# Kernel tuning notes

Hardware: AMD Instinct MI355X
Metric: run time of the kernel (lower is better)

Reference implementation:

```python
import jax, jax.numpy as jnp
import numpy as np

D_MODEL = 1024
N_HEADS = 16
N_KV = 4
HEAD_DIM = 64
R = 256
B, N = 2, 2048


def setup_inputs() -> dict:
    key = jax.random.key(0)
    ks = jax.random.split(key, 5)
    x = jax.random.normal(ks[0], (B, N, D_MODEL), jnp.float32)
    # rotary cos/sin table: (N, HEAD_DIM//2, 2)
    inv = 1.0 / (10000.0 ** (jnp.arange(0, HEAD_DIM, 2, dtype=jnp.float32) / HEAD_DIM))
    ang = jnp.arange(N, dtype=jnp.float32)[:, None] * inv[None, :]
    freqs_cis = jnp.stack([jnp.cos(ang), jnp.sin(ang)], axis=-1)
    s = 0.02
    Wq = jax.random.normal(ks[1], (D_MODEL, N_HEADS * HEAD_DIM), jnp.float32) * s
    Wk = jax.random.normal(ks[2], (D_MODEL, N_KV * HEAD_DIM), jnp.float32) * s
    Wv = jax.random.normal(ks[3], (D_MODEL, N_KV * HEAD_DIM), jnp.float32) * s
    Wo = jax.random.normal(ks[4], (N_HEADS * HEAD_DIM, D_MODEL), jnp.float32) * s
    return dict(x=x, freqs_cis=freqs_cis, Wq=Wq, Wk=Wk, Wv=Wv, Wo=Wo)


def _select_pairs(scores_i, best_b_i, r):
    """Greedy top-r pair selection with unique-b constraint (one batch row)."""
    half = scores_i.shape[0]
    order = jnp.argsort(-scores_i)  # descending by best similarity

    def step(carry, a_local):
        used, count = carry
        b_local = best_b_i[a_local]
        take = jnp.logical_and(jnp.logical_not(used[b_local]), count < r)
        used = used.at[b_local].set(used[b_local] | take)
        count = count + take.astype(jnp.int32)
        return (used, count), (take, a_local.astype(jnp.int32), b_local.astype(jnp.int32))

    (_, count), (takes, a_locs, b_locs) = jax.lax.scan(
        step, (jnp.zeros(half, bool), jnp.int32(0)), order)
    pos = jnp.cumsum(takes.astype(jnp.int32)) - 1
    idx = jnp.where(takes, pos, r)  # dump non-taken into slot r
    sel_a = jnp.zeros(r + 1, jnp.int32).at[idx].set(a_locs)[:r]
    sel_b = jnp.zeros(r + 1, jnp.int32).at[idx].set(b_locs)[:r]
    valid = jnp.arange(r) < count  # pad (if fewer than r unique) with first pair
    sel_a = jnp.where(valid, sel_a, sel_a[0])
    sel_b = jnp.where(valid, sel_b, sel_b[0])
    return sel_a, sel_b


def bipartite_indices(metric, r):
    """Returns (global_a, global_b, keep_idx) for merge/unmerge."""
    Bm, Nm, _ = metric.shape
    a = metric[:, 0::2]  # (B, half, C)
    b = metric[:, 1::2]
    an = a / jnp.maximum(jnp.linalg.norm(a, axis=-1, keepdims=True), 1e-12)
    bn = b / jnp.maximum(jnp.linalg.norm(b, axis=-1, keepdims=True), 1e-12)
    scores = jnp.einsum('bic,bjc->bij', an, bn)  # (B, half, half)
    best_scores = scores.max(axis=2)
    best_b = scores.argmax(axis=2)
    sel_a, sel_b = jax.vmap(lambda s, m: _select_pairs(s, m, r))(best_scores, best_b)
    global_a = 2 * sel_a      # even indices
    global_b = 2 * sel_b + 1  # odd indices
    bidx = jnp.arange(Bm)[:, None]
    keep_mask = jnp.ones((Bm, Nm), bool).at[bidx, global_b].set(False)
    # stable argsort puts kept (False) positions first, in original order
    keep_idx = jnp.argsort(~keep_mask, axis=1)[:, :Nm - r]
    return global_a, global_b, keep_idx


def merge(x, global_a, global_b, keep_idx):
    Bm = x.shape[0]
    bidx = jnp.arange(Bm)[:, None]
    xa = jnp.take_along_axis(x, global_a[..., None], axis=1)
    xb = jnp.take_along_axis(x, global_b[..., None], axis=1)
    x_out = x.at[bidx, global_a].set((xa + xb) * 0.5)
    return jnp.take_along_axis(x_out, keep_idx[..., None], axis=1)


def unmerge(xm, global_a, global_b, keep_idx, n_orig):
    Bm, _, C = xm.shape
    bidx = jnp.arange(Bm)[:, None]
    out = jnp.zeros((Bm, n_orig, C), xm.dtype).at[bidx, keep_idx].set(xm)
    xa = jnp.take_along_axis(out, global_a[..., None], axis=1)
    return out.at[bidx, global_b].set(xa)


def _rope(t, freqs):
    # t: (B, N, H, HD), freqs: (N, HD//2, 2)
    cos = freqs[None, :, None, :, 0]
    sin = freqs[None, :, None, :, 1]
    t1 = t[..., 0::2]
    t2 = t[..., 1::2]
    rot = jnp.stack([t1 * cos - t2 * sin, t1 * sin + t2 * cos], axis=-1)
    return rot.reshape(t.shape)


def _attention(x_m, freqs, Wq, Wk, Wv, Wo):
    Bm, Nm, _ = x_m.shape
    q = (x_m @ Wq).reshape(Bm, Nm, N_HEADS, HEAD_DIM)
    k = (x_m @ Wk).reshape(Bm, Nm, N_KV, HEAD_DIM)
    v = (x_m @ Wv).reshape(Bm, Nm, N_KV, HEAD_DIM)
    q = _rope(q, freqs)
    k = _rope(k, freqs)
    rep = N_HEADS // N_KV
    k = jnp.repeat(k, rep, axis=2)
    v = jnp.repeat(v, rep, axis=2)
    att = jnp.einsum('bqhd,bkhd->bhqk', q, k) / np.sqrt(HEAD_DIM).astype(np.float32)
    w = jax.nn.softmax(att, axis=-1)
    o = jnp.einsum('bhqk,bkhd->bqhd', w, v).reshape(Bm, Nm, N_HEADS * HEAD_DIM)
    return o @ Wo


def reference(x, freqs_cis, Wq, Wk, Wv, Wo):
    n = x.shape[1]
    metric = jax.lax.stop_gradient(x @ Wk)  # k_proj under no_grad
    ga, gb, ki = bipartite_indices(metric, R)
    x_m = merge(x, ga, gb, ki)
    n_merged = x_m.shape[1]
    out_m = _attention(x_m, freqs_cis[:n_merged], Wq, Wk, Wv, Wo)
    return unmerge(out_m, ga, gb, ki, n)
```

## Files before the change

### kernel.cpp

```cpp
#include <hip/hip_runtime.h>
#include <hip/hip_bf16.h>
#include <math.h>

#define BB 2
#define NN 2048
#define DM 1024
#define NH 16
#define NKV 4
#define HD 64
#define RR 256
#define HALF 1024
#define NM 1792
#define NT 28
#define NSPL 4

typedef __bf16 bf16x8 __attribute__((ext_vector_type(8)));
typedef float f32x4 __attribute__((ext_vector_type(4)));

__device__ inline unsigned pk2(float a, float b) {
  union { __bf16 h; unsigned short u; } ua, ub;
  ua.h = (__bf16)a;
  ub.h = (__bf16)b;
  return (unsigned)ua.u | ((unsigned)ub.u << 16);
}

__device__ inline unsigned shu(unsigned v, int s) {
  return (unsigned)__shfl((int)v, s, 64);
}

__device__ __forceinline__ void async16(const void* g, void* l) {
  __builtin_amdgcn_global_load_lds(
      (const __attribute__((address_space(1))) void*)g,
      (__attribute__((address_space(3))) void*)l, 16, 0, 0);
}

__global__ __launch_bounds__(256) void gemm_bf16(
    const __bf16* __restrict__ A, const __bf16* __restrict__ Bt,
    float* __restrict__ C, int M, int N, int K) {
  __shared__ __align__(16) __bf16 As[8192];
  __shared__ __align__(16) __bf16 Bs[4096];
  const int bm0 = blockIdx.x * 128;
  const int bn0 = blockIdx.y * 64;
  const int w = threadIdx.x >> 6;
  const int lane = threadIdx.x & 63;
  f32x4 acc[2][4];
#pragma unroll
  for (int i = 0; i < 2; ++i)
#pragma unroll
    for (int nt = 0; nt < 4; ++nt) acc[i][nt] = (f32x4){0.f, 0.f, 0.f, 0.f};
  for (int kk = 0; kk < K; kk += 64) {
    __syncthreads();
#pragma unroll
    for (int it = 0; it < 4; ++it) {
      const int c = it * 256 + w * 64 + lane;
      async16(A + (size_t)(bm0 + ((c >> 7) << 4) + (c & 15)) * K + kk +
                  (((c >> 6) & 1) << 5) + (((c >> 4) & 3) << 3),
              &As[(it * 256 + w * 64) * 8]);
    }
#pragma unroll
    for (int it = 0; it < 2; ++it) {
      const int c = it * 256 + w * 64 + lane;
      async16(Bt + (size_t)(bn0 + ((c >> 7) << 4) + (c & 15)) * K + kk +
                  (((c >> 6) & 1) << 5) + (((c >> 4) & 3) << 3),
              &Bs[(it * 256 + w * 64) * 8]);
    }
    __syncthreads();
#pragma unroll
    for (int s = 0; s < 2; ++s) {
      bf16x8 a0 = *(const bf16x8*)&As[((2 * w) * 128 + s * 64 + lane) * 8];
      bf16x8 a1 = *(const bf16x8*)&As[((2 * w + 1) * 128 + s * 64 + lane) * 8];
#pragma unroll
      for (int nt = 0; nt < 4; ++nt) {
        bf16x8 bfr = *(const bf16x8*)&Bs[(nt * 128 + s * 64 + lane) * 8];
        acc[0][nt] =
            __builtin_amdgcn_mfma_f32_16x16x32_bf16(a0, bfr, acc[0][nt], 0, 0, 0);
        acc[1][nt] =
            __builtin_amdgcn_mfma_f32_16x16x32_bf16(a1, bfr, acc[1][nt], 0, 0, 0);
      }
    }
  }
  const int g = lane >> 4, ml = lane & 15;
#pragma unroll
  for (int i = 0; i < 2; ++i)
#pragma unroll
    for (int nt = 0; nt < 4; ++nt)
#pragma unroll
      for (int r = 0; r < 4; ++r)
        C[(size_t)(bm0 + (2 * w + i) * 16 + g * 4 + r) * N + bn0 + nt * 16 +
          ml] = acc[i][nt][r];
}

__global__ __launch_bounds__(256) void gemm_wo(
    const __bf16* __restrict__ A, const __bf16* __restrict__ Bt,
    const int* __restrict__ keep_idx, const int* __restrict__ dst2,
    float* __restrict__ out, int M, int N, int K) {
  __shared__ __align__(16) __bf16 As[8192];
  __shared__ __align__(16) __bf16 Bs[4096];
  const int bm0 = blockIdx.x * 128;
  const int bn0 = blockIdx.y * 64;
  const int w = threadIdx.x >> 6;
  const int lane = threadIdx.x & 63;
  f32x4 acc[2][4];
#pragma unroll
  for (int i = 0; i < 2; ++i)
#pragma unroll
    for (int nt = 0; nt < 4; ++nt) acc[i][nt] = (f32x4){0.f, 0.f, 0.f, 0.f};
  for (int kk = 0; kk < K; kk += 64) {
    __syncthreads();
#pragma unroll
    for (int it = 0; it < 4; ++it) {
      const int c = it * 256 + w * 64 + lane;
      async16(A + (size_t)(bm0 + ((c >> 7) << 4) + (c & 15)) * K + kk +
                  (((c >> 6) & 1) << 5) + (((c >> 4) & 3) << 3),
              &As[(it * 256 + w * 64) * 8]);
    }
#pragma unroll
    for (int it = 0; it < 2; ++it) {
      const int c = it * 256 + w * 64 + lane;
      async16(Bt + (size_t)(bn0 + ((c >> 7) << 4) + (c & 15)) * K + kk +
                  (((c >> 6) & 1) << 5) + (((c >> 4) & 3) << 3),
              &Bs[(it * 256 + w * 64) * 8]);
    }
    __syncthreads();
#pragma unroll
    for (int s = 0; s < 2; ++s) {
      bf16x8 a0 = *(const bf16x8*)&As[((2 * w) * 128 + s * 64 + lane) * 8];
      bf16x8 a1 = *(const bf16x8*)&As[((2 * w + 1) * 128 + s * 64 + lane) * 8];
#pragma unroll
      for (int nt = 0; nt < 4; ++nt) {
        bf16x8 bfr = *(const bf16x8*)&Bs[(nt * 128 + s * 64 + lane) * 8];
        acc[0][nt] =
            __builtin_amdgcn_mfma_f32_16x16x32_bf16(a0, bfr, acc[0][nt], 0, 0, 0);
        acc[1][nt] =
            __builtin_amdgcn_mfma_f32_16x16x32_bf16(a1, bfr, acc[1][nt], 0, 0, 0);
      }
    }
  }
  const int g = lane >> 4, ml = lane & 15;
#pragma unroll
  for (int i = 0; i < 2; ++i)
#pragma unroll
    for (int r = 0; r < 4; ++r) {
      const int row = bm0 + (2 * w + i) * 16 + g * 4 + r;
      const int bb = row / NM, tt = row % NM;
      const int p1 = keep_idx[bb * NM + tt];
      const int p2 = dst2[bb * NM + tt];
#pragma unroll
      for (int nt = 0; nt < 4; ++nt) {
        const int col = bn0 + nt * 16 + ml;
        float v = acc[i][nt][r];
        out[((size_t)(bb * NN + p1)) * DM + col] = v;
        if (p2 >= 0) out[((size_t)(bb * NN + p2)) * DM + col] = v;
      }
    }
}

__global__ __launch_bounds__(256) void gemm3t(
    const __bf16* __restrict__ Ah, const __bf16* __restrict__ Al,
    const __bf16* __restrict__ Bh, const __bf16* __restrict__ Bl,
    float* __restrict__ C0, float* __restrict__ C1, int M, int N, int K) {
  __shared__ __align__(16) __bf16 Ahs[4096], Als[4096], Bhs[4096], Bls[4096];
  const int z = blockIdx.z;
  float* C = z ? C1 : C0;
  const int kof = z * (K / 2);
  const int bm0 = blockIdx.x * 64;
  const int bn0 = blockIdx.y * 64;
  const int w = threadIdx.x >> 6;
  const int lane = threadIdx.x & 63;
  f32x4 acc[4];
#pragma unroll
  for (int nt = 0; nt < 4; ++nt) acc[nt] = (f32x4){0.f, 0.f, 0.f, 0.f};
  for (int kk = kof; kk < kof + K / 2; kk += 64) {
    __syncthreads();
#pragma unroll
    for (int it = 0; it < 2; ++it) {
      const int c = it * 256 + w * 64 + lane;
      const size_t ra = (size_t)(bm0 + ((c >> 7) << 4) + (c & 15)) * K;
      const size_t rb = (size_t)(bn0 + ((c >> 7) << 4) + (c & 15)) * K;
      const int col = kk + (((c >> 6) & 1) << 5) + (((c >> 4) & 3) << 3);
      const int lb = (it * 256 + w * 64) * 8;
      async16(Ah + ra + col, &Ahs[lb]);
      async16(Al + ra + col, &Als[lb]);
      async16(Bh + rb + col, &Bhs[lb]);
      async16(Bl + rb + col, &Bls[lb]);
    }
    __syncthreads();
#pragma unroll
    for (int s = 0; s < 2; ++s) {
      bf16x8 ah = *(const bf16x8*)&Ahs[((w * 2 + s) * 64 + lane) * 8];
      bf16x8 al = *(const bf16x8*)&Als[((w * 2 + s) * 64 + lane) * 8];
#pragma unroll
      for (int nt = 0; nt < 4; ++nt) {
        bf16x8 bh = *(const bf16x8*)&Bhs[((nt * 2 + s) * 64 + lane) * 8];
        bf16x8 bl = *(const bf16x8*)&Bls[((nt * 2 + s) * 64 + lane) * 8];
        acc[nt] = __builtin_amdgcn_mfma_f32_16x16x32_bf16(al, bh, acc[nt], 0, 0, 0);
        acc[nt] = __builtin_amdgcn_mfma_f32_16x16x32_bf16(ah, bl, acc[nt], 0, 0, 0);
        acc[nt] = __builtin_amdgcn_mfma_f32_16x16x32_bf16(ah, bh, acc[nt], 0, 0, 0);
      }
    }
  }
  const int g = lane >> 4, ml = lane & 15;
#pragma unroll
  for (int nt = 0; nt < 4; ++nt)
#pragma unroll
    for (int r = 0; r < 4; ++r)
      C[(size_t)(bm0 + w * 16 + g * 4 + r) * N + bn0 + nt * 16 + ml] =
          acc[nt][r];
}

__global__ __launch_bounds__(256) void gemm_scam(
    const __bf16* __restrict__ Ah, const __bf16* __restrict__ Al,
    const __bf16* __restrict__ Bh, const __bf16* __restrict__ Bl,
    float* __restrict__ sval, int* __restrict__ sidx) {
  __shared__ __align__(16) __bf16 Ahs[4096], Als[4096], Bhs[4096], Bls[4096];
  const size_t zo = (size_t)blockIdx.z * HALF * 256;
  const int bm0 = blockIdx.x * 64;
  const int bn0 = blockIdx.y * 64;
  const int w = threadIdx.x >> 6;
  const int lane = threadIdx.x & 63;
  f32x4 acc[4];
#pragma unroll
  for (int nt = 0; nt < 4; ++nt) acc[nt] = (f32x4){0.f, 0.f, 0.f, 0.f};
  for (int kk = 0; kk < 256; kk += 64) {
    __syncthreads();
#pragma unroll
    for (int it = 0; it < 2; ++it) {
      const int c = it * 256 + w * 64 + lane;
      const size_t ra = zo + (size_t)(bm0 + ((c >> 7) << 4) + (c & 15)) * 256;
      const size_t rb = zo + (size_t)(bn0 + ((c >> 7) << 4) + (c & 15)) * 256;
      const int col = kk + (((c >> 6) & 1) << 5) + (((c >> 4) & 3) << 3);
      const int lb = (it * 256 + w * 64) * 8;
      async16(Ah + ra + col, &Ahs[lb]);
      async16(Al + ra + col, &Als[lb]);
      async16(Bh + rb + col, &Bhs[lb]);
      async16(Bl + rb + col, &Bls[lb]);
    }
    __syncthreads();
#pragma unroll
    for (int s = 0; s < 2; ++s) {
      bf16x8 ah = *(const bf16x8*)&Ahs[((w * 2 + s) * 64 + lane) * 8];
      bf16x8 al = *(const bf16x8*)&Als[((w * 2 + s) * 64 + lane) * 8];
#pragma unroll
      for (int nt = 0; nt < 4; ++nt) {
        bf16x8 bh = *(const bf16x8*)&Bhs[((nt * 2 + s) * 64 + lane) * 8];
        bf16x8 bl = *(const bf16x8*)&Bls[((nt * 2 + s) * 64 + lane) * 8];
        acc[nt] = __builtin_amdgcn_mfma_f32_16x16x32_bf16(al, bh, acc[nt], 0, 0, 0);
        acc[nt] = __builtin_amdgcn_mfma_f32_16x16x32_bf16(ah, bl, acc[nt], 0, 0, 0);
        acc[nt] = __builtin_amdgcn_mfma_f32_16x16x32_bf16(ah, bh, acc[nt], 0, 0, 0);
      }
    }
  }
  const int g = lane >> 4, ml = lane & 15;
#pragma unroll
  for (int r = 0; r < 4; ++r) {
    float bv = acc[0][r];
    int bc = bn0 + ml;
#pragma unroll
    for (int nt = 1; nt < 4; ++nt) {
      float v = acc[nt][r];
      int c = bn0 + nt * 16 + ml;
      if (v > bv) { bv = v; bc = c; }
    }
#pragma unroll
    for (int off = 1; off < 16; off <<= 1) {
      float vo = __shfl_xor(bv, off, 64);
      int co = __shfl_xor(bc, off, 64);
      if (vo > bv || (vo == bv && co < bc)) { bv = vo; bc = co; }
    }
    if (ml == 0) {
      const int row = bm0 + w * 16 + g * 4 + r;
      const size_t o = ((size_t)blockIdx.z * HALF + row) * 16 + (bn0 >> 6);
      sval[o] = bv;
      sidx[o] = bc;
    }
  }
}

__global__ __launch_bounds__(256) void prep_in(
    const float* __restrict__ Wq, const float* __restrict__ Wk,
    const float* __restrict__ Wv, const float* __restrict__ Wo,
    const float* __restrict__ x, __bf16* __restrict__ Wqkvt,
    __bf16* __restrict__ Wktl, __bf16* __restrict__ Wot,
    __bf16* __restrict__ xh, __bf16* __restrict__ xl) {
  const int z = blockIdx.x;
  if (z >= 640) {
    const int i = (z - 640) * 256 + threadIdx.x;
    float4 v = ((const float4*)x)[i];
    float f[4] = {v.x, v.y, v.z, v.w};
    union { __bf16 h[4]; uint2 u; } H, L;
#pragma unroll
    for (int j = 0; j < 4; ++j) {
      __bf16 hh = (__bf16)f[j];
      H.h[j] = hh;
      L.h[j] = (__bf16)(f[j] - (float)hh);
    }
    ((uint2*)xh)[i] = H.u;
    ((uint2*)xl)[i] = L.u;
    return;
  }
  __shared__ float ld[64][65];
  const float* src;
  __bf16* dsth;
  __bf16* dstl = nullptr;
  int N, k0, n0, rowoff;
  if (z < 256) {
    src = Wq; N = 1024; k0 = (z >> 4) << 6; n0 = (z & 15) << 6;
    dsth = Wqkvt; rowoff = 0;
  } else if (z < 320) {
    int zz = z - 256;
    src = Wk; N = 256; k0 = (zz >> 2) << 6; n0 = (zz & 3) << 6;
    dsth = Wqkvt; rowoff = 1024; dstl = Wktl;
  } else if (z < 384) {
    int zz = z - 320;
    src = Wv; N = 256; k0 = (zz >> 2) << 6; n0 = (zz & 3) << 6;
    dsth = Wqkvt; rowoff = 1280;
  } else {
    int zz = z - 384;
    src = Wo; N = 1024; k0 = (zz >> 4) << 6; n0 = (zz & 15) << 6;
    dsth = Wot; rowoff = 0;
  }
  for (int i = threadIdx.x; i < 1024; i += 256) {
    int r = i >> 4, c4 = i & 15;
    float4 v = *(const float4*)(src + (size_t)(k0 + r) * N + n0 + c4 * 4);
    ld[r][c4 * 4 + 0] = v.x;
    ld[r][c4 * 4 + 1] = v.y;
    ld[r][c4 * 4 + 2] = v.z;
    ld[r][c4 * 4 + 3] = v.w;
  }
  __syncthreads();
  for (int i = threadIdx.x; i < 4096; i += 256) {
    int n = i >> 6, k = i & 63;
    float v = ld[k][n];
    __bf16 hh = (__bf16)v;
    dsth[(size_t)(rowoff + n0 + n) * 1024 + k0 + k] = hh;
    if (dstl)
      dstl[(size_t)(n0 + n) * 1024 + k0 + k] = (__bf16)(v - (float)hh);
  }
}

__global__ __launch_bounds__(256) void normalize_split(
    const float* __restrict__ m0, const float* __restrict__ m1,
    __bf16* __restrict__ anh, __bf16* __restrict__ anl,
    __bf16* __restrict__ bnh, __bf16* __restrict__ bnl) {
  const int row = blockIdx.x;
  const int b = row >> 11;
  const int r = row & 2047;
  const int t = threadIdx.x;
  float v = m0[(size_t)row * 256 + t] + m1[(size_t)row * 256 + t];
  float ss = v * v;
#pragma unroll
  for (int o = 32; o > 0; o >>= 1) ss += __shfl_xor(ss, o, 64);
  __shared__ float wsum[4];
  if ((t & 63) == 0) wsum[t >> 6] = ss;
  __syncthreads();
  float tot = wsum[0] + wsum[1] + wsum[2] + wsum[3];
  float inv = 1.f / fmaxf(sqrtf(tot), 1e-12f);
  float nv = v * inv;
  __bf16 hh = (__bf16)nv;
  __bf16 ll = (__bf16)(nv - (float)hh);
  size_t o = ((size_t)b * HALF + (r >> 1)) * 256 + t;
  if (r & 1) {
    bnh[o] = hh;
    bnl[o] = ll;
  } else {
    anh[o] = hh;
    anl[o] = ll;
  }
}

__global__ __launch_bounds__(512) void sort_desc(
    const float* __restrict__ sval, const int* __restrict__ sidx,
    int* __restrict__ best_b, int* __restrict__ order) {
  const int b = blockIdx.x;
  __shared__ float sv[1024];
  __shared__ int si[1024];
  for (int i = threadIdx.x; i < 1024; i += 512) {
    const size_t base = ((size_t)b * HALF + i) * 16;
    float bv = sval[base];
    int bc = sidx[base];
#pragma unroll
    for (int e = 1; e < 16; ++e) {
      float v = sval[base + e];
      int c = sidx[base + e];
      if (v > bv || (v == bv && c < bc)) { bv = v; bc = c; }
    }
    sv[i] = bv;
    si[i] = i;
    best_b[b * HALF + i] = bc;
  }
  __syncthreads();
  for (int k = 2; k <= 1024; k <<= 1) {
    for (int j = k >> 1; j > 0; j >>= 1) {
      for (int t = threadIdx.x; t < 1024; t += 512) {
        int ixj = t ^ j;
        if (ixj > t) {
          bool dir = ((t & k) == 0);
          float va = sv[t], vb = sv[ixj];
          int ia = si[t], ib = si[ixj];
          bool before = (vb > va) || (vb == va && ib < ia);
          if (before == dir) {
            sv[t] = vb; sv[ixj] = va;
            si[t] = ib; si[ixj] = ia;
          }
        }
      }
      __syncthreads();
    }
  }
  for (int i = threadIdx.x; i < 1024; i += 512) order[b * HALF + i] = si[i];
}

__global__ __launch_bounds__(256) void select_and_index(
    const int* __restrict__ best_b, const int* __restrict__ order,
    int* __restrict__ keep_idx, int* __restrict__ partner,
    int* __restrict__ dst2) {
  const int b = blockIdx.x;
  __shared__ int rankA[HALF];
  __shared__ int minrank[HALF];
  __shared__ int taken[HALF];
  __shared__ int sel_a[RR], sel_b[RR];
  __shared__ int removed[NN];
  __shared__ int src_row[NN];
  __shared__ int tsum[256];
  const int t = threadIdx.x;

  for (int i = t; i < HALF; i += 256) { minrank[i] = 0x7fffffff; taken[i] = 0; }
  for (int i = t; i < NN; i += 256) {
    removed[i] = 0;
    partner[b * NN + i] = -1;
  }
  for (int i = t; i < NM; i += 256) dst2[b * NM + i] = -1;
  __syncthreads();
  int ord[4];
#pragma unroll
  for (int q = 0; q < 4; ++q) {
    int step = t * 4 + q;
    ord[q] = order[b * HALF + step];
    rankA[ord[q]] = step;
  }
  __syncthreads();
#pragma unroll
  for (int q = 0; q < 4; ++q) {
    int a = t * 4 + q;
    atomicMin(&minrank[best_b[b * HALF + a]], rankA[a]);
  }
  __syncthreads();
  for (int i = t; i < HALF; i += 256) {
    int mr = minrank[i];
    if (mr != 0x7fffffff) taken[mr] = 1;
  }
  __syncthreads();
  int c[4];
  int mysum = 0;
#pragma unroll
  for (int q = 0; q < 4; ++q) { c[q] = taken[t * 4 + q]; mysum += c[q]; }
  tsum[t] = mysum;
  __syncthreads();
  for (int off = 1; off < 256; off <<= 1) {
    int v = (t >= off) ? tsum[t - off] : 0;
    __syncthreads();
    tsum[t] += v;
    __syncthreads();
  }
  int run = tsum[t] - mysum;
#pragma unroll
  for (int q = 0; q < 4; ++q) {
    if (c[q] && run < RR) {
      int a = ord[q];
      sel_a[run] = 2 * a;
      sel_b[run] = 2 * best_b[b * HALF + a] + 1;
    }
    run += c[q];
  }
  __syncthreads();
  const int cnt = min(tsum[255], RR);
  if (t >= cnt) { sel_a[t] = sel_a[0]; sel_b[t] = sel_b[0]; }
  __syncthreads();
  {
    int ga = sel_a[t], gb = sel_b[t];
    removed[gb] = 1;
    partner[b * NN + ga] = gb;
  }
  __syncthreads();
  int myc = 0;
#pragma unroll
  for (int q = 0; q < 8; ++q) myc += !removed[8 * t + q];
  tsum[t] = myc;
  __syncthreads();
  for (int off = 1; off < 256; off <<= 1) {
    int v = (t >= off) ? tsum[t - off] : 0;
    __syncthreads();
    tsum[t] += v;
    __syncthreads();
  }
  int pos = tsum[t] - myc;
#pragma unroll
  for (int q = 0; q < 8; ++q) {
    int p = 8 * t + q;
    int sr = -1;
    if (!removed[p]) {
      if (pos < NM) {
        keep_idx[b * NM + pos] = p;
        sr = pos;
      }
      ++pos;
    }
    src_row[p] = sr;
  }
  __syncthreads();
  {
    int sr = src_row[sel_a[t]];
    dst2[b * NM + sr] = sel_b[t];
  }
}

__global__ __launch_bounds__(256) void merge_kernel(
    const float* __restrict__ x, const int* __restrict__ keep_idx,
    const int* __restrict__ partner, __bf16* __restrict__ x_mb) {
  const int mrow = blockIdx.x;
  const int b = mrow / NM;
  const int t = mrow % NM;
  const int p = keep_idx[b * NM + t];
  const int pp = partner[b * NN + p];
  const float4* src =
      reinterpret_cast<const float4*>(x + ((size_t)b * NN + p) * DM);
  float4 val = src[threadIdx.x];
  if (pp >= 0) {
    const float4* s2 =
        reinterpret_cast<const float4*>(x + ((size_t)b * NN + pp) * DM);
    float4 v2 = s2[threadIdx.x];
    val.x = 0.5f * (val.x + v2.x);
    val.y = 0.5f * (val.y + v2.y);
    val.z = 0.5f * (val.z + v2.z);
    val.w = 0.5f * (val.w + v2.w);
  }
  union { __bf16 h[4]; uint2 u; } U;
  U.h[0] = (__bf16)val.x;
  U.h[1] = (__bf16)val.y;
  U.h[2] = (__bf16)val.z;
  U.h[3] = (__bf16)val.w;
  ((uint2*)(x_mb + (size_t)mrow * DM))[threadIdx.x] = U.u;
}

__global__ __launch_bounds__(256) void prep_qkv(
    const float* __restrict__ qkv, const float* __restrict__ fc,
    __bf16* __restrict__ qbh, __bf16* __restrict__ kbh,
    __bf16* __restrict__ vtb) {
  __shared__ float ld[64][65];
  const int z = blockIdx.x;
  if (z < BB * NM) {
    const int row = z;
    const int t = row % NM;
    const int b = row / NM;
    for (int idx = threadIdx.x; idx < 640; idx += 256) {
      int u = idx & 31;
      float c = fc[(t * 32 + u) * 2];
      float s = fc[(t * 32 + u) * 2 + 1];
      if (idx < 512) {
        int h = idx >> 5;
        const float* p = qkv + (size_t)row * 1536 + h * 64 + 2 * u;
        float x1 = p[0], x2 = p[1];
        __bf16* d = qbh + ((size_t)(b * NH + h) * NM + t) * 64 + 2 * u;
        d[0] = (__bf16)((x1 * c - x2 * s) * 0.125f);
        d[1] = (__bf16)((x1 * s + x2 * c) * 0.125f);
      } else {
        int h = (idx - 512) >> 5;
        const float* p = qkv + (size_t)row * 1536 + 1024 + h * 64 + 2 * u;
        float x1 = p[0], x2 = p[1];
        __bf16* d = kbh + ((size_t)(b * NKV + h) * NM + t) * 64 + 2 * u;
        d[0] = (__bf16)(x1 * c - x2 * s);
        d[1] = (__bf16)(x1 * s + x2 * c);
      }
    }
    return;
  }
  int bid = z - BB * NM;
  const int kt = bid % (NM / 64); bid /= (NM / 64);
  const int kvh = bid % NKV;
  const int b = bid / NKV;
  const int j0 = kt * 64;
  for (int t2 = threadIdx.x; t2 < 1024; t2 += 256) {
    int key = t2 >> 4, c4 = t2 & 15;
    float4 v4 = *reinterpret_cast<const float4*>(
        qkv + (size_t)(b * NM + j0 + key) * 1536 + 1280 + kvh * 64 + c4 * 4);
    ld[key][c4 * 4 + 0] = v4.x;
    ld[key][c4 * 4 + 1] = v4.y;
    ld[key][c4 * 4 + 2] = v4.z;
    ld[key][c4 * 4 + 3] = v4.w;
  }
  __syncthreads();
  const int dim = threadIdx.x >> 2, kc = threadIdx.x & 3;
  __bf16* out = vtb + ((size_t)(b * NKV + kvh) * 64 + dim) * NM + j0 + kc * 16;
#pragma unroll
  for (int kk = 0; kk < 16; ++kk) out[kk] = (__bf16)ld[kc * 16 + kk][dim];
}

__global__ __launch_bounds__(256) void attn_mfma(
    const __bf16* __restrict__ qbh, const __bf16* __restrict__ kbh,
    const __bf16* __restrict__ vtb, float* __restrict__ pl,
    __bf16* __restrict__ pacc) {
  __shared__ __align__(16) __bf16 Ks[4096];
  __shared__ __align__(16) __bf16 Vs[4096];
  int bid = blockIdx.x;
  const int qt1 = bid % (NM / 16); bid /= (NM / 16);
  const int split = bid % NSPL; bid /= NSPL;
  const int kvh = bid % NKV;
  const int b = bid / NKV;
  const int w = threadIdx.x >> 6;
  const int lane = threadIdx.x & 63;
  const int h = kvh * 4 + w;
  const int qt = qt1 * 16;
  const int g = lane >> 4;
  const int ml = lane & 15;

  const __bf16* qrow = qbh + ((size_t)(b * NH + h) * NM + qt + ml) * 64;
  bf16x8 qa0 = *reinterpret_cast<const bf16x8*>(qrow + g * 8);
  bf16x8 qa1 = *reinterpret_cast<const bf16x8*>(qrow + 32 + g * 8);

  f32x4 acc[4];
#pragma unroll
  for (int mt = 0; mt < 4; ++mt) acc[mt] = (f32x4){0.f, 0.f, 0.f, 0.f};
  float lsum = 0.f;

  const __bf16* kp = kbh + (size_t)(b * NKV + kvh) * NM * 64;
  const __bf16* vp = vtb + (size_t)(b * NKV + kvh) * 64 * NM;
  const int src0 = ((lane >> 4) & 1) * 32 + ml;
  const int src1 = src0 + 16;
  const int sel = g >> 1;

  const int jt0 = split * (NT / NSPL);
  for (int jt = jt0; jt < jt0 + NT / NSPL; ++jt) {
    __syncthreads();
#pragma unroll
    for (int it = 0; it < 2; ++it) {
      const int c = it * 256 + w * 64 + lane;
      const int lb = (it * 256 + w * 64) * 8;
      async16(kp + (size_t)(jt * 64 + ((c >> 7) << 4) + (c & 15)) * 64 +
                  (((c >> 6) & 1) << 5) + (((c >> 4) & 3) << 3),
              &Ks[lb]);
      async16(vp + (size_t)(((c >> 7) << 4) + (c & 15)) * NM + jt * 64 +
                  (((c >> 6) & 1) << 5) + (((c >> 4) & 3) << 3),
              &Vs[lb]);
    }
    __syncthreads();
    f32x4 S[4];
#pragma unroll
    for (int nt = 0; nt < 4; ++nt) {
      bf16x8 k0 = *(const bf16x8*)&Ks[(nt * 128 + lane) * 8];
      bf16x8 k1 = *(const bf16x8*)&Ks[(nt * 128 + 64 + lane) * 8];
      f32x4 s4 = (f32x4){0.f, 0.f, 0.f, 0.f};
      s4 = __builtin_amdgcn_mfma_f32_16x16x32_bf16(k0, qa0, s4, 0, 0, 0);
      s4 = __builtin_amdgcn_mfma_f32_16x16x32_bf16(k1, qa1, s4, 0, 0, 0);
      S[nt] = s4;
    }
    float p[4][4];
#pragma unroll
    for (int nt = 0; nt < 4; ++nt)
#pragma unroll
      for (int r = 0; r < 4; ++r) {
        p[nt][r] = __expf(S[nt][r]);
        lsum += p[nt][r];
      }
    unsigned pk[4][2];
#pragma unroll
    for (int nt = 0; nt < 4; ++nt) {
      pk[nt][0] = pk2(p[nt][0], p[nt][1]);
      pk[nt][1] = pk2(p[nt][2], p[nt][3]);
    }
    unsigned A00 = shu(pk[0][0], src0), A01 = shu(pk[0][1], src0);
    unsigned A10 = shu(pk[1][0], src0), A11 = shu(pk[1][1], src0);
    unsigned B00 = shu(pk[0][0], src1), B01 = shu(pk[0][1], src1);
    unsigned B10 = shu(pk[1][0], src1), B11 = shu(pk[1][1], src1);
    unsigned C00 = shu(pk[2][0], src0), C01 = shu(pk[2][1], src0);
    unsigned C10 = shu(pk[3][0], src0), C11 = shu(pk[3][1], src0);
    unsigned D00 = shu(pk[2][0], src1), D01 = shu(pk[2][1], src1);
    unsigned D10 = shu(pk[3][0], src1), D11 = shu(pk[3][1], src1);
    union { uint4 u; bf16x8 v; } P0, P1;
    P0.u.x = sel ? A10 : A00; P0.u.y = sel ? A11 : A01;
    P0.u.z = sel ? B10 : B00; P0.u.w = sel ? B11 : B01;
    P1.u.x = sel ? C10 : C00; P1.u.y = sel ? C11 : C01;
    P1.u.z = sel ? D10 : D00; P1.u.w = sel ? D11 : D01;
#pragma unroll
    for (int mt = 0; mt < 4; ++mt) {
      bf16x8 v0 = *(const bf16x8*)&Vs[(mt * 128 + lane) * 8];
      bf16x8 v1 = *(const bf16x8*)&Vs[(mt * 128 + 64 + lane) * 8];
      acc[mt] = __builtin_amdgcn_mfma_f32_16x16x32_bf16(v0, P0.v, acc[mt], 0, 0, 0);
      acc[mt] = __builtin_amdgcn_mfma_f32_16x16x32_bf16(v1, P1.v, acc[mt], 0, 0, 0);
    }
  }
  lsum += __shfl_xor(lsum, 16, 64);
  lsum += __shfl_xor(lsum, 32, 64);
  const size_t row = (size_t)(b * NH + h) * NM + qt + ml;
  if (g == 0) pl[row * NSPL + split] = lsum;
  __bf16* pa = pacc + (row * NSPL + split) * 64;
#pragma unroll
  for (int mt = 0; mt < 4; ++mt) {
    uint2 u;
    u.x = pk2(acc[mt][0], acc[mt][1]);
    u.y = pk2(acc[mt][2], acc[mt][3]);
    *reinterpret_cast<uint2*>(pa + mt * 16 + g * 4) = u;
  }
}

__global__ __launch_bounds__(256) void attn_combine(
    const float* __restrict__ pl, const __bf16* __restrict__ pacc,
    __bf16* __restrict__ attn_ob) {
  const size_t rid = (size_t)blockIdx.x * 4 + (threadIdx.x >> 6);
  const int d = threadIdx.x & 63;
  float num = 0.f, den = 0.f;
#pragma unroll
  for (int s = 0; s < NSPL; ++s) {
    num += (float)pacc[(rid * NSPL + s) * 64 + d];
    den += pl[rid * NSPL + s];
  }
  float o = num / den;
  const int q = (int)(rid % NM);
  const int h = (int)((rid / NM) % NH);
  const int b = (int)(rid / ((size_t)NM * NH));
  attn_ob[((size_t)(b * NM + q)) * DM + h * 64 + d] = (__bf16)o;
}

extern "C" void kernel_launch(void* const* d_in, const int* in_sizes, int n_in,
                              void* d_out, int out_size, void* d_ws,
                              size_t ws_size, hipStream_t stream) {
  const float* x = (const float*)d_in[0];
  const float* fc = (const float*)d_in[1];
  const float* Wq = (const float*)d_in[2];
  const float* Wk = (const float*)d_in[3];
  const float* Wv = (const float*)d_in[4];
  const float* Wo = (const float*)d_in[5];
  float* out = (float*)d_out;

  char* ws = (char*)d_ws;
  size_t off = 0;
  auto alloc = [&](size_t bytes) {
    void* p = ws + off;
    off += (bytes + 255) & ~(size_t)255;
    return p;
  };
  float* metric0 = (float*)alloc((size_t)BB * NN * 256 * 4);
  float* metric1 = (float*)alloc((size_t)BB * NN * 256 * 4);
  int* best_b = (int*)alloc((size_t)BB * HALF * 4);
  int* order = (int*)alloc((size_t)BB * HALF * 4);
  int* keep_idx = (int*)alloc((size_t)BB * NM * 4);
  int* partner = (int*)alloc((size_t)BB * NN * 4);
  int* dst2 = (int*)alloc((size_t)BB * NM * 4);
  float* sval = (float*)alloc((size_t)BB * HALF * 16 * 4);
  int* sidx = (int*)alloc((size_t)BB * HALF * 16 * 4);
  char* bigreg = (char*)alloc((size_t)30 * 1024 * 1024);
  __bf16* xh = (__bf16*)bigreg;
  __bf16* xl = (__bf16*)(bigreg + (size_t)8704 * 1024);
  __bf16* anh = (__bf16*)bigreg;
  __bf16* anl = (__bf16*)(bigreg + (size_t)1100 * 1024);
  __bf16* bnh = (__bf16*)(bigreg + (size_t)2200 * 1024);
  __bf16* bnl = (__bf16*)(bigreg + (size_t)3300 * 1024);
  float* qkv = (float*)bigreg;
  __bf16* pacc = (__bf16*)bigreg;
  __bf16* x_mb = (__bf16*)alloc((size_t)BB * NM * DM * 2);
  __bf16* qbh = (__bf16*)alloc((size_t)BB * NH * NM * 64 * 2);
  __bf16* kbh = (__bf16*)alloc((size_t)BB * NKV * NM * 64 * 2);
  __bf16* vtb = (__bf16*)alloc((size_t)BB * NKV * 64 * NM * 2);
  __bf16* attn_ob = (__bf16*)alloc((size_t)BB * NM * DM * 2);
  float* pl = (float*)alloc((size_t)BB * NH * NM * NSPL * 4);
  __bf16* Wqkvt = (__bf16*)alloc((size_t)1536 * DM * 2);
  __bf16* Wktl = (__bf16*)alloc((size_t)256 * DM * 2);
  __bf16* Wot = (__bf16*)alloc((size_t)DM * DM * 2);
  const __bf16* Wkth = Wqkvt + (size_t)1024 * 1024;

  prep_in<<<640 + (BB * NN * DM / 4) / 256, 256, 0, stream>>>(
      Wq, Wk, Wv, Wo, x, Wqkvt, Wktl, Wot, xh, xl);
  gemm3t<<<dim3(64, 4, 2), 256, 0, stream>>>(xh, xl, Wkth, Wktl, metric0,
                                             metric1, BB * NN, 256, DM);
  normalize_split<<<BB * NN, 256, 0, stream>>>(metric0, metric1, anh, anl, bnh,
                                               bnl);
  gemm_scam<<<dim3(16, 16, 2), 256, 0, stream>>>(anh, anl, bnh, bnl, sval,
                                                 sidx);
  sort_desc<<<BB, 512, 0, stream>>>(sval, sidx, best_b, order);
  select_and_index<<<BB, 256, 0, stream>>>(best_b, order, keep_idx, partner,
                                           dst2);
  merge_kernel<<<BB * NM, 256, 0, stream>>>(x, keep_idx, partner, x_mb);
  gemm_bf16<<<dim3(28, 24), 256, 0, stream>>>(x_mb, Wqkvt, qkv, BB * NM, 1536,
                                              DM);
  prep_qkv<<<BB * NM + BB * NKV * (NM / 64), 256, 0, stream>>>(qkv, fc, qbh,
                                                               kbh, vtb);
  attn_mfma<<<BB * NKV * NSPL * (NM / 16), 256, 0, stream>>>(qbh, kbh, vtb, pl,
                                                             pacc);
  attn_combine<<<(BB * NH * NM) / 4, 256, 0, stream>>>(pl, pacc, attn_ob);
  gemm_wo<<<dim3(28, 16), 256, 0, stream>>>(attn_ob, Wot, keep_idx, dst2, out,
                                            BB * NM, DM, DM);
}
```

Before: 300.9 us.

## Double query rows per attention block and transpose P through LDS

The attention kernel now runs 512 threads per block, with two 16-row query tiles sharing each K/V tile loaded into shared memory. This halves the K/V global-to-LDS traffic per query and halves the grid size. The 16 cross-lane shuffles and selects that relaid the probability matrix are replaced by a padded per-wave LDS scratch: each lane writes its packed results and reads back the operand layout the MFMA needs. In exchange the block uses more LDS and has fewer, larger blocks, which may lower occupancy.

New measurement: 286.5 us. -4.8%, faster.

```diff
diff --git a/kernel.cpp b/kernel.cpp
--- a/kernel.cpp
+++ b/kernel.cpp
@@ -22,10 +22,6 @@
   ua.h = (__bf16)a;
   ub.h = (__bf16)b;
   return (unsigned)ua.u | ((unsigned)ub.u << 16);
-}
-
-__device__ inline unsigned shu(unsigned v, int s) {
-  return (unsigned)__shfl((int)v, s, 64);
 }
 
 __device__ __forceinline__ void async16(const void* g, void* l) {
@@ -595,23 +591,27 @@
   for (int kk = 0; kk < 16; ++kk) out[kk] = (__bf16)ld[kc * 16 + kk][dim];
 }
 
-__global__ __launch_bounds__(256) void attn_mfma(
+#define LDP 72
+
+__global__ __launch_bounds__(512) void attn_mfma(
     const __bf16* __restrict__ qbh, const __bf16* __restrict__ kbh,
     const __bf16* __restrict__ vtb, float* __restrict__ pl,
     __bf16* __restrict__ pacc) {
   __shared__ __align__(16) __bf16 Ks[4096];
   __shared__ __align__(16) __bf16 Vs[4096];
+  __shared__ __align__(16) __bf16 Pt[8 * 16 * LDP];
   int bid = blockIdx.x;
-  const int qt1 = bid % (NM / 16); bid /= (NM / 16);
+  const int qt2 = bid % (NM / 32); bid /= (NM / 32);
   const int split = bid % NSPL; bid /= NSPL;
   const int kvh = bid % NKV;
   const int b = bid / NKV;
   const int w = threadIdx.x >> 6;
   const int lane = threadIdx.x & 63;
-  const int h = kvh * 4 + w;
-  const int qt = qt1 * 16;
+  const int h = kvh * 4 + (w & 3);
+  const int qt = qt2 * 32 + (w >> 2) * 16;
   const int g = lane >> 4;
   const int ml = lane & 15;
+  __bf16* Pw = Pt + w * 16 * LDP;
 
   const __bf16* qrow = qbh + ((size_t)(b * NH + h) * NM + qt + ml) * 64;
   bf16x8 qa0 = *reinterpret_cast<const bf16x8*>(qrow + g * 8);
@@ -624,17 +624,13 @@
 
   const __bf16* kp = kbh + (size_t)(b * NKV + kvh) * NM * 64;
   const __bf16* vp = vtb + (size_t)(b * NKV + kvh) * 64 * NM;
-  const int src0 = ((lane >> 4) & 1) * 32 + ml;
-  const int src1 = src0 + 16;
-  const int sel = g >> 1;
 
   const int jt0 = split * (NT / NSPL);
   for (int jt = jt0; jt < jt0 + NT / NSPL; ++jt) {
     __syncthreads();
-#pragma unroll
-    for (int it = 0; it < 2; ++it) {
-      const int c = it * 256 + w * 64 + lane;
-      const int lb = (it * 256 + w * 64) * 8;
+    {
+      const int c = threadIdx.x;
+      const int lb = w * 512;
       async16(kp + (size_t)(jt * 64 + ((c >> 7) << 4) + (c & 15)) * 64 +
                   (((c >> 6) & 1) << 5) + (((c >> 4) & 3) << 3),
               &Ks[lb]);
@@ -653,39 +649,26 @@
       s4 = __builtin_amdgcn_mfma_f32_16x16x32_bf16(k1, qa1, s4, 0, 0, 0);
       S[nt] = s4;
     }
-    float p[4][4];
-#pragma unroll
-    for (int nt = 0; nt < 4; ++nt)
-#pragma unroll
-      for (int r = 0; r < 4; ++r) {
-        p[nt][r] = __expf(S[nt][r]);
-        lsum += p[nt][r];
-      }
-    unsigned pk[4][2];
 #pragma unroll
     for (int nt = 0; nt < 4; ++nt) {
-      pk[nt][0] = pk2(p[nt][0], p[nt][1]);
-      pk[nt][1] = pk2(p[nt][2], p[nt][3]);
-    }
-    unsigned A00 = shu(pk[0][0], src0), A01 = shu(pk[0][1], src0);
-    unsigned A10 = shu(pk[1][0], src0), A11 = shu(pk[1][1], src0);
-    unsigned B00 = shu(pk[0][0], src1), B01 = shu(pk[0][1], src1);
-    unsigned B10 = shu(pk[1][0], src1), B11 = shu(pk[1][1], src1);
-    unsigned C00 = shu(pk[2][0], src0), C01 = shu(pk[2][1], src0);
-    unsigned C10 = shu(pk[3][0], src0), C11 = shu(pk[3][1], src0);
-    unsigned D00 = shu(pk[2][0], src1), D01 = shu(pk[2][1], src1);
-    unsigned D10 = shu(pk[3][0], src1), D11 = shu(pk[3][1], src1);
-    union { uint4 u; bf16x8 v; } P0, P1;
-    P0.u.x = sel ? A10 : A00; P0.u.y = sel ? A11 : A01;
-    P0.u.z = sel ? B10 : B00; P0.u.w = sel ? B11 : B01;
-    P1.u.x = sel ? C10 : C00; P1.u.y = sel ? C11 : C01;
-    P1.u.z = sel ? D10 : D00; P1.u.w = sel ? D11 : D01;
+      float p0 = __expf(S[nt][0]);
+      float p1 = __expf(S[nt][1]);
+      float p2 = __expf(S[nt][2]);
+      float p3 = __expf(S[nt][3]);
+      lsum += (p0 + p1) + (p2 + p3);
+      uint2 u;
+      u.x = pk2(p0, p1);
+      u.y = pk2(p2, p3);
+      *reinterpret_cast<uint2*>(&Pw[ml * LDP + nt * 16 + g * 4]) = u;
+    }
+    bf16x8 P0 = *(const bf16x8*)&Pw[ml * LDP + g * 8];
+    bf16x8 P1 = *(const bf16x8*)&Pw[ml * LDP + 32 + g * 8];
 #pragma unroll
     for (int mt = 0; mt < 4; ++mt) {
       bf16x8 v0 = *(const bf16x8*)&Vs[(mt * 128 + lane) * 8];
       bf16x8 v1 = *(const bf16x8*)&Vs[(mt * 128 + 64 + lane) * 8];
-      acc[mt] = __builtin_amdgcn_mfma_f32_16x16x32_bf16(v0, P0.v, acc[mt], 0, 0, 0);
-      acc[mt] = __builtin_amdgcn_mfma_f32_16x16x32_bf16(v1, P1.v, acc[mt], 0, 0, 0);
+      acc[mt] = __builtin_amdgcn_mfma_f32_16x16x32_bf16(v0, P0, acc[mt], 0, 0, 0);
+      acc[mt] = __builtin_amdgcn_mfma_f32_16x16x32_bf16(v1, P1, acc[mt], 0, 0, 0);
     }
   }
   lsum += __shfl_xor(lsum, 16, 64);
@@ -783,7 +766,7 @@
                                               DM);
   prep_qkv<<<BB * NM + BB * NKV * (NM / 64), 256, 0, stream>>>(qkv, fc, qbh,
                                                                kbh, vtb);
-  attn_mfma<<<BB * NKV * NSPL * (NM / 16), 256, 0, stream>>>(qbh, kbh, vtb, pl,
+  attn_mfma<<<BB * NKV * NSPL * (NM / 32), 512, 0, stream>>>(qbh, kbh, vtb, pl,
                                                              pacc);
   attn_combine<<<(BB * NH * NM) / 4, 256, 0, stream>>>(pl, pacc, attn_ob);
   gemm_wo<<<dim3(28, 16), 256, 0, stream>>>(attn_ob, Wot, keep_idx, dst2, out,
```
